# Optimization experiments

Hardware: AMD Instinct MI355X
Metric: run time of the kernel (lower is better)

## Reference

```python
import jax, jax.numpy as jnp
import numpy as np

B, L, D, NHEADS, P = 64, 256, 768, 8, 3
VOCAB, DEP, NLAYERS = 30522, 45, 2
LAM = 0.5


def _forward(src_mask, aspect_mask, lex, attention_mask,
             tok_emb, seg_emb, pool_w, pool_b, ln_a, ln_b,
             dep_emb, fc1_w, fc1_b, fc2_w, fc2_b,
             aq_w, aq_b, ak_w, ak_b, lq_w, lq_b, lk_w, lk_b, root_w,
             gcn_w, gcn_b, fc3_w, fc3_b, cls_w, cls_b, vlin_w,
             text_bert_indices, bert_segments_ids, ori_tag, head):
    b, l = text_bert_indices.shape
    d = tok_emb.shape[1]
    dk = d // NHEADS
    NEG = jnp.float32(-1e30)
    # stand-in BERT encoder: token + segment embeddings, tanh pooler on [CLS]
    seq = tok_emb[text_bert_indices] + seg_emb[bert_segments_ids]
    pooled = jnp.tanh(seq[:, 0] @ pool_w + pool_b)
    # torch LayerNorm variant: unbiased std (ddof=1)
    mean = seq.mean(-1, keepdims=True)
    std = jnp.std(seq, axis=-1, keepdims=True, ddof=1)
    gcn_in = ln_a * (seq - mean) / (std + 1e-6) + ln_b
    # in-place fmask[:,0]=1 mutates src_mask storage in torch -> effective mask
    sm = src_mask.at[:, 0].set(1.0)
    # dependency-tag score -> per-token softmax -> scatter into [L,L] adjacency
    dep_h = jax.nn.relu(dep_emb[ori_tag] @ fc1_w + fc1_b)
    dep_s = (dep_h @ fc2_w + fc2_b)[..., 0]                      # [B,L]
    dep_feat = jax.nn.softmax(dep_s * sm + (1.0 - sm) * NEG, axis=1)
    to_idx = jnp.arange(1, l)
    fro = head[:, :l - 1]                                        # [B,L-1]
    b_idx = jnp.arange(b)[:, None]
    vals = dep_feat[:, :l - 1]
    dep_adj = jnp.ones((b, l, l), jnp.float32)
    dep_adj = dep_adj.at[b_idx, fro, to_idx[None, :]].set(vals)
    dep_adj = dep_adj.at[b_idx, to_idx[None, :], fro].set(vals)
    # multi-head attention-as-adjacency (returns softmax weights only)
    q = (gcn_in @ aq_w + aq_b).reshape(b, l, NHEADS, dk).transpose(0, 2, 1, 3)
    k = (gcn_in @ ak_w + ak_b).reshape(b, l, NHEADS, dk).transpose(0, 2, 1, 3)
    scores = jnp.einsum('bhqd,bhkd->bhqk', q, k) / (jnp.sqrt(jnp.float32(dk)) + 1e-9)
    scores = jnp.where(sm[:, None, None, :] == 0, jnp.float32(-1e9), scores)
    adj_ag = jax.nn.softmax(scores, axis=-1).mean(axis=1)        # [B,L,L]
    eye = jnp.eye(l, dtype=jnp.float32)
    adj_ag = (adj_ag * (1.0 - eye) + eye) * sm[:, :, None]
    # structured latent attention (stand-in for missing StructuredAtt):
    # masked bilinear attention biased by dep_adj + root attention loss
    q2 = gcn_in @ lq_w + lq_b
    k2 = gcn_in @ lk_w + lk_b
    lat = jnp.einsum('bqd,bkd->bqk', q2, k2) / jnp.sqrt(jnp.float32(d))
    lat = lat + dep_adj + (1.0 - sm)[:, None, :] * (-10000.0)
    adj_latent = jax.nn.softmax(lat, axis=-1)
    root_p = jax.nn.softmax((gcn_in @ root_w)[..., 0] * sm + (1.0 - sm) * NEG, axis=1)
    loss_root = -jnp.mean(jnp.log(jnp.sum(root_p * aspect_mask, axis=1) + 1e-9))
    adj_latent = (adj_latent * (1.0 - eye) + eye) * sm[:, :, None]
    # gated dual-adjacency GCN layers
    H_l = gcn_in
    I_sem = gcn_in
    for layer in range(gcn_w.shape[0]):
        g_l = jax.nn.sigmoid(H_l)
        I_sem = (adj_ag @ H_l) @ gcn_w[layer] + gcn_b[layer]
        I_lat = (adj_latent @ H_l) @ gcn_w[layer] + gcn_b[layer]
        g = jax.nn.sigmoid(I_lat)
        lam_g = LAM * g
        I_com = (1.0 - lam_g) * I_sem + lam_g * I_lat
        H_out = jax.nn.relu(I_com @ fc3_w + fc3_b)
        H_l = g_l * H_out + (1.0 - g_l) * H_l
    # readout
    asp_wn = aspect_mask.sum(axis=1, keepdims=True)              # [B,1]
    m3 = sm[:, :, None]
    h_l = H_l * m3
    h_sem = I_sem * m3
    beta = jnp.einsum('bqd,bkd->bqk', h_l, h_sem) / 1000.0
    attn_o = jax.nn.softmax(beta.sum(axis=1, keepdims=True), axis=2)  # [B,1,L]
    outputs = (attn_o @ I_sem)[:, 0]                             # [B,D]
    sem_pool = (I_sem * aspect_mask[:, :, None]).sum(axis=1) / (asp_wn + 1e-9)
    final = jnp.concatenate([outputs, sem_pool, pooled], axis=-1)  # [B,3D]
    logits = final @ cls_w + cls_b
    e = (H_l @ vlin_w)[..., 0]
    lw = jax.nn.softmax(e, axis=1) * 50.0
    lw = lw * sm.at[:, 0].set(0.0)
    lexicon_loss = jnp.mean((lw - lex) ** 2)
    return logits, loss_root, lexicon_loss


def setup_inputs() -> dict:
    key = jax.random.key(0)
    ks = jax.random.split(key, 24)
    s = 0.02
    n = lambda i, shape: jax.random.normal(ks[i], shape, dtype=jnp.float32) * s
    inp = {}
    inp['text_bert_indices'] = jax.random.randint(ks[0], (B, L), 0, VOCAB, dtype=jnp.int32)
    inp['bert_segments_ids'] = jnp.zeros((B, L), jnp.int32)
    inp['attention_mask'] = jnp.ones((B, L), jnp.float32)
    inp['src_mask'] = jnp.ones((B, L), jnp.float32)
    inp['aspect_mask'] = jax.random.randint(ks[1], (B, L), 0, 2).astype(jnp.float32)
    inp['lex'] = jax.random.uniform(ks[2], (B, L), dtype=jnp.float32)
    inp['ori_tag'] = jax.random.randint(ks[3], (B, L), 0, DEP, dtype=jnp.int32)
    inp['head'] = jax.random.randint(ks[4], (B, L), 0, L, dtype=jnp.int32)
    inp['tok_emb'] = n(5, (VOCAB, D)); inp['seg_emb'] = n(6, (2, D))
    inp['pool_w'] = n(7, (D, D)); inp['pool_b'] = jnp.zeros((D,), jnp.float32)
    inp['ln_a'] = jnp.ones((D,), jnp.float32); inp['ln_b'] = jnp.zeros((D,), jnp.float32)
    inp['dep_emb'] = n(8, (DEP, 300))
    inp['fc1_w'] = n(9, (300, 256)); inp['fc1_b'] = jnp.zeros((256,), jnp.float32)
    inp['fc2_w'] = n(10, (256, 1)); inp['fc2_b'] = jnp.zeros((1,), jnp.float32)
    inp['aq_w'] = n(11, (D, D)); inp['aq_b'] = jnp.zeros((D,), jnp.float32)
    inp['ak_w'] = n(12, (D, D)); inp['ak_b'] = jnp.zeros((D,), jnp.float32)
    inp['lq_w'] = n(13, (D, D)); inp['lq_b'] = jnp.zeros((D,), jnp.float32)
    inp['lk_w'] = n(14, (D, D)); inp['lk_b'] = jnp.zeros((D,), jnp.float32)
    inp['root_w'] = n(15, (D, 1))
    inp['gcn_w'] = n(16, (NLAYERS, D, D)); inp['gcn_b'] = jnp.zeros((NLAYERS, D), jnp.float32)
    inp['fc3_w'] = n(17, (D, D)); inp['fc3_b'] = jnp.zeros((D,), jnp.float32)
    inp['cls_w'] = n(18, (3 * D, P)); inp['cls_b'] = jnp.zeros((P,), jnp.float32)
    inp['vlin_w'] = n(19, (D, 1))
    return inp


def reference(text_bert_indices, bert_segments_ids, attention_mask, src_mask, aspect_mask, lex,
              ori_tag, head, tok_emb, seg_emb, pool_w, pool_b, ln_a, ln_b, dep_emb,
              fc1_w, fc1_b, fc2_w, fc2_b, aq_w, aq_b, ak_w, ak_b, lq_w, lq_b, lk_w, lk_b,
              root_w, gcn_w, gcn_b, fc3_w, fc3_b, cls_w, cls_b, vlin_w):
    return _forward(src_mask, aspect_mask, lex, attention_mask,
                    tok_emb, seg_emb, pool_w, pool_b, ln_a, ln_b,
                    dep_emb, fc1_w, fc1_b, fc2_w, fc2_b,
                    aq_w, aq_b, ak_w, ak_b, lq_w, lq_b, lk_w, lk_b, root_w,
                    gcn_w, gcn_b, fc3_w, fc3_b, cls_w, cls_b, vlin_w,
                    text_bert_indices, bert_segments_ids, ori_tag, head)
```

## Files before the change

kernel.cpp:

```cpp
#include <hip/hip_runtime.h>
#include <hip/hip_bf16.h>
#include <math.h>

#define DI __device__ __forceinline__

constexpr int cB = 64, cL = 256, cD = 768;
constexpr long BLD = (long)cB * cL * cD;
constexpr long BLL = (long)cB * cL * cL;
constexpr long cLL = (long)cL * cL;
constexpr long cLD = (long)cL * cD;

typedef __attribute__((ext_vector_type(8))) short b8;
typedef __attribute__((ext_vector_type(4))) float f4;

DI float wsum(float v) {
#pragma unroll
  for (int o = 32; o > 0; o >>= 1) v += __shfl_down(v, o, 64);
  return v;
}
DI float wsum_all(float v) {
#pragma unroll
  for (int m = 32; m > 0; m >>= 1) v += __shfl_xor(v, m, 64);
  return v;
}
DI float wmax_all(float v) {
#pragma unroll
  for (int m = 32; m > 0; m >>= 1) v = fmaxf(v, __shfl_xor(v, m, 64));
  return v;
}
DI float wmaxr(float v) {
#pragma unroll
  for (int o = 32; o > 0; o >>= 1) v = fmaxf(v, __shfl_down(v, o, 64));
  return v;
}
DI float blockSum(float v) {
  __shared__ float sh[4];
  v = wsum(v);
  __syncthreads();
  if ((threadIdx.x & 63) == 0) sh[threadIdx.x >> 6] = v;
  __syncthreads();
  return sh[0] + sh[1] + sh[2] + sh[3];
}
DI float blockMax(float v) {
  __shared__ float sh[4];
  v = wmaxr(v);
  __syncthreads();
  if ((threadIdx.x & 63) == 0) sh[threadIdx.x >> 6] = v;
  __syncthreads();
  return fmaxf(fmaxf(sh[0], sh[1]), fmaxf(sh[2], sh[3]));
}
DI float sigf(float x) { return 1.f / (1.f + expf(-x)); }

template <int OBF, int RELU, int BIAS, int EPI>
__global__ __launch_bounds__(256, 2) void bgemm(
    const __hip_bfloat16* __restrict__ A, const __hip_bfloat16* __restrict__ BT,
    void* __restrict__ Cv, const float* __restrict__ bias,
    float* __restrict__ auxf, __hip_bfloat16* __restrict__ auxb,
    int K, int lda, int ldb, int ldc,
    int zshift, int zmask, long sA1, long sA2, long sB1, long sB2, long sC,
    int czdiv) {
  __shared__ __hip_bfloat16 Asp[4 * 129 * 8];
  __shared__ __hip_bfloat16 Bsp[4 * 129 * 8];
  int z = blockIdx.z;
  A += (long)(z >> zshift) * sA1 + (long)(z & zmask) * sA2;
  BT += (long)(z >> zshift) * sB1 + (long)(z & zmask) * sB2;
  int tid = threadIdx.x;
  int lane = tid & 63, w = tid >> 6;
  int wr = w >> 1, wc = w & 1;
  int l16 = lane & 15, q = lane >> 4;
  int m0 = blockIdx.y << 7, n0 = blockIdx.x << 7;

  int fm = tid >> 2, fq = tid & 3;
  const __hip_bfloat16* Ap0 = A + (long)(m0 + fm) * lda + fq * 8;
  const __hip_bfloat16* Ap1 = A + (long)(m0 + fm + 64) * lda + fq * 8;
  const __hip_bfloat16* Bp0 = BT + (long)(n0 + fm) * ldb + fq * 8;
  const __hip_bfloat16* Bp1 = BT + (long)(n0 + fm + 64) * ldb + fq * 8;
  __hip_bfloat16* Aw0 = &Asp[(fq * 129 + fm) * 8];
  __hip_bfloat16* Aw1 = &Asp[(fq * 129 + fm + 64) * 8];
  __hip_bfloat16* Bw0 = &Bsp[(fq * 129 + fm) * 8];
  __hip_bfloat16* Bw1 = &Bsp[(fq * 129 + fm + 64) * 8];

  f4 acc[4][4];
#pragma unroll
  for (int i = 0; i < 4; i++)
#pragma unroll
    for (int j = 0; j < 4; j++) acc[i][j] = (f4){0.f, 0.f, 0.f, 0.f};

  b8 pa0 = *(const b8*)Ap0, pa1 = *(const b8*)Ap1;
  b8 pb0 = *(const b8*)Bp0, pb1 = *(const b8*)Bp1;
  for (int k0 = 0; k0 < K; k0 += 32) {
    __syncthreads();
    *(b8*)Aw0 = pa0; *(b8*)Aw1 = pa1;
    *(b8*)Bw0 = pb0; *(b8*)Bw1 = pb1;
    __syncthreads();
    int k1 = k0 + 32;
    if (k1 < K) {
      pa0 = *(const b8*)(Ap0 + k1); pa1 = *(const b8*)(Ap1 + k1);
      pb0 = *(const b8*)(Bp0 + k1); pb1 = *(const b8*)(Bp1 + k1);
    }
    b8 af[4], bf[4];
#pragma unroll
    for (int i = 0; i < 4; i++)
      af[i] = *(const b8*)&Asp[(q * 129 + wr * 64 + i * 16 + l16) * 8];
#pragma unroll
    for (int j = 0; j < 4; j++)
      bf[j] = *(const b8*)&Bsp[(q * 129 + wc * 64 + j * 16 + l16) * 8];
#pragma unroll
    for (int i = 0; i < 4; i++)
#pragma unroll
      for (int j = 0; j < 4; j++)
        acc[i][j] = __builtin_amdgcn_mfma_f32_16x16x32_bf16(af[i], bf[j], acc[i][j], 0, 0, 0);
  }
  if (EPI == 4) {
#pragma unroll
    for (int j = 0; j < 4; j++) {
      int n = n0 + wc * 64 + j * 16 + l16;
#pragma unroll
      for (int i = 0; i < 4; i++) {
        int m = m0 + wr * 64 + i * 16 + (q << 2);
        __hip_bfloat16 t4[4];
#pragma unroll
        for (int r = 0; r < 4; r++) t4[r] = __float2bfloat16(acc[i][j][r]);
        long bidx = (long)(m >> 8) * sC + (long)n * cL + (m & 255);
        *(uint2*)&((__hip_bfloat16*)Cv)[bidx] = *(uint2*)t4;
      }
    }
    return;
  }
  long cz = (long)(z >> czdiv) * sC;
#pragma unroll
  for (int j = 0; j < 4; j++) {
    int n = n0 + wc * 64 + j * 16 + l16;
    float bv = BIAS ? bias[n] : 0.f;
#pragma unroll
    for (int i = 0; i < 4; i++) {
#pragma unroll
      for (int r = 0; r < 4; r++) {
        int m = m0 + wr * 64 + i * 16 + q * 4 + r;
        long idx = cz + (long)m * ldc + n;
        float v = acc[i][j][r] + bv;
        if (EPI == 0) {
          if (RELU) v = fmaxf(v, 0.f);
          if (OBF)
            ((__hip_bfloat16*)Cv)[idx] = __float2bfloat16(v);
          else
            ((float*)Cv)[idx] = v;
        } else if (EPI == 3) {
          atomicAdd(&((float*)Cv)[idx], v);
        } else {
          v = fmaxf(v, 0.f);
          float h = auxf[idx];
          float g = sigf(h);
          float o = h + g * (v - h);
          auxf[idx] = o;
          auxb[idx] = __float2bfloat16(o);
        }
      }
    }
  }
}

__global__ __launch_bounds__(256, 2) void bgemm_dual(
    const __hip_bfloat16* __restrict__ A1g, const __hip_bfloat16* __restrict__ A2g,
    const __hip_bfloat16* __restrict__ BTg, float* __restrict__ IsemF,
    __hip_bfloat16* __restrict__ Icb, const float* __restrict__ bias,
    int write_isem) {
  __shared__ __hip_bfloat16 A1sp[4 * 129 * 8];
  __shared__ __hip_bfloat16 A2sp[4 * 129 * 8];
  __shared__ __hip_bfloat16 Bsp[4 * 129 * 8];
  int z = blockIdx.z;
  const __hip_bfloat16* A1 = A1g + (long)z * cLL;
  const __hip_bfloat16* A2 = A2g + (long)z * cLL;
  const __hip_bfloat16* BT = BTg + (long)z * cLD;
  int tid = threadIdx.x;
  int lane = tid & 63, w = tid >> 6;
  int wr = w >> 1, wc = w & 1;
  int l16 = lane & 15, q = lane >> 4;
  int m0 = blockIdx.y << 7, n0 = blockIdx.x << 7;

  int fm = tid >> 2, fq = tid & 3;
  const __hip_bfloat16* A1p0 = A1 + (long)(m0 + fm) * cL + fq * 8;
  const __hip_bfloat16* A1p1 = A1p0 + 64L * cL;
  const __hip_bfloat16* A2p0 = A2 + (long)(m0 + fm) * cL + fq * 8;
  const __hip_bfloat16* A2p1 = A2p0 + 64L * cL;
  const __hip_bfloat16* Bp0 = BT + (long)(n0 + fm) * cL + fq * 8;
  const __hip_bfloat16* Bp1 = Bp0 + 64L * cL;
  __hip_bfloat16* w10 = &A1sp[(fq * 129 + fm) * 8];
  __hip_bfloat16* w11 = &A1sp[(fq * 129 + fm + 64) * 8];
  __hip_bfloat16* w20 = &A2sp[(fq * 129 + fm) * 8];
  __hip_bfloat16* w21 = &A2sp[(fq * 129 + fm + 64) * 8];
  __hip_bfloat16* wb0 = &Bsp[(fq * 129 + fm) * 8];
  __hip_bfloat16* wb1 = &Bsp[(fq * 129 + fm + 64) * 8];

  f4 ac1[4][4], ac2[4][4];
#pragma unroll
  for (int i = 0; i < 4; i++)
#pragma unroll
    for (int j = 0; j < 4; j++) {
      ac1[i][j] = (f4){0.f, 0.f, 0.f, 0.f};
      ac2[i][j] = (f4){0.f, 0.f, 0.f, 0.f};
    }

  b8 p10 = *(const b8*)A1p0, p11 = *(const b8*)A1p1;
  b8 p20 = *(const b8*)A2p0, p21 = *(const b8*)A2p1;
  b8 pb0 = *(const b8*)Bp0, pb1 = *(const b8*)Bp1;
  for (int k0 = 0; k0 < cL; k0 += 32) {
    __syncthreads();
    *(b8*)w10 = p10; *(b8*)w11 = p11;
    *(b8*)w20 = p20; *(b8*)w21 = p21;
    *(b8*)wb0 = pb0; *(b8*)wb1 = pb1;
    __syncthreads();
    int k1 = k0 + 32;
    if (k1 < cL) {
      p10 = *(const b8*)(A1p0 + k1); p11 = *(const b8*)(A1p1 + k1);
      p20 = *(const b8*)(A2p0 + k1); p21 = *(const b8*)(A2p1 + k1);
      pb0 = *(const b8*)(Bp0 + k1); pb1 = *(const b8*)(Bp1 + k1);
    }
    b8 a1f[4], a2f[4], bf[4];
#pragma unroll
    for (int i = 0; i < 4; i++) {
      a1f[i] = *(const b8*)&A1sp[(q * 129 + wr * 64 + i * 16 + l16) * 8];
      a2f[i] = *(const b8*)&A2sp[(q * 129 + wr * 64 + i * 16 + l16) * 8];
    }
#pragma unroll
    for (int j = 0; j < 4; j++)
      bf[j] = *(const b8*)&Bsp[(q * 129 + wc * 64 + j * 16 + l16) * 8];
#pragma unroll
    for (int i = 0; i < 4; i++)
#pragma unroll
      for (int j = 0; j < 4; j++) {
        ac1[i][j] = __builtin_amdgcn_mfma_f32_16x16x32_bf16(a1f[i], bf[j], ac1[i][j], 0, 0, 0);
        ac2[i][j] = __builtin_amdgcn_mfma_f32_16x16x32_bf16(a2f[i], bf[j], ac2[i][j], 0, 0, 0);
      }
  }
  long cz = (long)z * cLD;
#pragma unroll
  for (int j = 0; j < 4; j++) {
    int n = n0 + wc * 64 + j * 16 + l16;
    float bv = bias[n];
#pragma unroll
    for (int i = 0; i < 4; i++) {
#pragma unroll
      for (int r = 0; r < 4; r++) {
        int m = m0 + wr * 64 + i * 16 + q * 4 + r;
        long idx = cz + (long)m * cD + n;
        float is = ac1[i][j][r] + bv;
        float il = ac2[i][j][r] + bv;
        float g = 0.5f * sigf(il);
        Icb[idx] = __float2bfloat16(is + g * (il - is));
        if (write_isem) IsemF[idx] = is;
      }
    }
  }
}

__global__ void k_wconv7(const float* __restrict__ s0, const float* __restrict__ s1,
                         const float* __restrict__ s2, const float* __restrict__ s3,
                         const float* __restrict__ s4, const float* __restrict__ s5,
                         const float* __restrict__ s6, __hip_bfloat16* __restrict__ dst) {
  const float* srcs[7] = {s0, s1, s2, s3, s4, s5, s6};
  const float* src = srcs[blockIdx.z];
  __hip_bfloat16* d = dst + (long)blockIdx.z * cD * cD;
  __shared__ float t[32][33];
  int k0 = blockIdx.x * 32, n0 = blockIdx.y * 32;
  int tx = threadIdx.x, ty = threadIdx.y;
#pragma unroll
  for (int i = 0; i < 32; i += 8) t[ty + i][tx] = src[(long)(k0 + ty + i) * cD + n0 + tx];
  __syncthreads();
#pragma unroll
  for (int i = 0; i < 32; i += 8)
    d[(long)(n0 + ty + i) * cD + k0 + tx] = __float2bfloat16(t[tx][ty + i]);
}

__global__ __launch_bounds__(256) void k_gcnin(
    const int* __restrict__ tbi, const int* __restrict__ bsi,
    const float* __restrict__ tok, const float* __restrict__ seg,
    const float* __restrict__ ln_a, const float* __restrict__ ln_b,
    const float* __restrict__ root_w,
    float* __restrict__ gcn_in, __hip_bfloat16* __restrict__ gib,
    float* __restrict__ x64, float* __restrict__ e1) {
  long bl = blockIdx.x;
  int t = tbi[bl], s = bsi[bl];
  const float* tr = tok + (long)t * cD;
  const float* sr = seg + (long)s * cD;
  float x[3];
  float ls = 0.f;
#pragma unroll
  for (int i = 0; i < 3; i++) {
    int d = threadIdx.x + (i << 8);
    x[i] = tr[d] + sr[d];
    ls += x[i];
  }
  if ((bl & 255) == 0) {
#pragma unroll
    for (int i = 0; i < 3; i++) x64[(bl >> 8) * cD + threadIdx.x + (i << 8)] = x[i];
  }
  float mean = blockSum(ls) * (1.f / 768.f);
  float lv = 0.f;
#pragma unroll
  for (int i = 0; i < 3; i++) { float c = x[i] - mean; lv += c * c; }
  float var = blockSum(lv) * (1.f / 767.f);
  float inv = 1.f / (sqrtf(var) + 1e-6f);
  float rdot = 0.f;
#pragma unroll
  for (int i = 0; i < 3; i++) {
    int d = threadIdx.x + (i << 8);
    float v = ln_a[d] * (x[i] - mean) * inv + ln_b[d];
    gcn_in[bl * cD + d] = v;
    gib[bl * cD + d] = __float2bfloat16(v);
    rdot += v * root_w[d];
  }
  float tot = blockSum(rdot);
  if (threadIdx.x == 0) e1[bl] = tot;
}

__global__ __launch_bounds__(256) void k_pool1(
    const float* __restrict__ x64, const float* __restrict__ pw,
    float* __restrict__ pacc) {
  __shared__ float pws[48][256];
  __shared__ float xs[16][48];
  int i0 = blockIdx.x * 48, j0 = blockIdx.y * 256, b0 = blockIdx.z * 16;
  for (int r = 0; r < 48; r++) pws[r][threadIdx.x] = pw[(long)(i0 + r) * cD + j0 + threadIdx.x];
  for (int idx = threadIdx.x; idx < 16 * 48; idx += 256)
    xs[idx / 48][idx % 48] = x64[(long)(b0 + idx / 48) * cD + i0 + idx % 48];
  __syncthreads();
  int j = threadIdx.x;
  for (int b = 0; b < 16; b++) {
    float acc = 0.f;
#pragma unroll 8
    for (int i = 0; i < 48; i++) acc += xs[b][i] * pws[i][j];
    atomicAdd(&pacc[(long)(b0 + b) * cD + j0 + j], acc);
  }
}
__global__ __launch_bounds__(256) void k_pool2(
    const float* __restrict__ pacc, const float* __restrict__ pb,
    float* __restrict__ pooled) {
  int b = blockIdx.x;
#pragma unroll
  for (int c = 0; c < 3; c++) {
    int j = (c << 8) + threadIdx.x;
    pooled[(long)b * cD + j] = tanhf(pacc[(long)b * cD + j] + pb[j]);
  }
}

__global__ __launch_bounds__(256) void k_s45(
    const float* __restrict__ dep_emb, const float* __restrict__ fc1w,
    const float* __restrict__ fc1b, const float* __restrict__ fc2w,
    const float* __restrict__ fc2b, float* __restrict__ s45) {
  int t = blockIdx.x;
  __shared__ float e[300];
  for (int i = threadIdx.x; i < 300; i += 256) e[i] = dep_emb[t * 300 + i];
  __syncthreads();
  int j = threadIdx.x;
  float h = fc1b[j];
  for (int i = 0; i < 300; i++) h += e[i] * fc1w[i * 256 + j];
  h = fmaxf(h, 0.f);
  float tot = blockSum(h * fc2w[j]);
  if (threadIdx.x == 0) s45[t] = tot + fc2b[0];
}

__global__ __launch_bounds__(256) void k_depfeat(
    const int* __restrict__ ori, const float* __restrict__ src_mask,
    const float* __restrict__ s45, float* __restrict__ dep_feat) {
  int b = blockIdx.x, l = threadIdx.x;
  float smv = (l == 0) ? 1.f : src_mask[b * cL + l];
  float sc = s45[ori[b * cL + l]] * smv + (1.f - smv) * (-1e30f);
  float mx = blockMax(sc);
  float ex = expf(sc - mx);
  float sum = blockSum(ex);
  dep_feat[b * cL + l] = ex / sum;
}

__global__ void k_bcat(const float* __restrict__ a, const float* __restrict__ b,
                       const float* __restrict__ c, const float* __restrict__ d,
                       float* __restrict__ o) {
  int i = blockIdx.x * 256 + threadIdx.x;
  float v = (i < 768) ? a[i] : (i < 1536) ? b[i - 768] : (i < 2304) ? c[i - 1536] : d[i - 2304];
  o[i] = v;
}

__global__ __launch_bounds__(256) void k_adjag_sm(
    const __hip_bfloat16* __restrict__ scores, const float* __restrict__ src_mask,
    __hip_bfloat16* __restrict__ adjag) {
  int b = blockIdx.x >> 8, i = blockIdx.x & 255;
  int tid = threadIdx.x, wave = tid >> 6, lane = tid & 63;
  __shared__ float accs[4][256];
  const float scale = 1.f / (sqrtf(96.f) + 1e-9f);
  float smj[4], acc[4];
#pragma unroll
  for (int c = 0; c < 4; c++) {
    int j = c * 64 + lane;
    smj[c] = (j == 0) ? 1.f : src_mask[b * cL + j];
    acc[c] = 0.f;
  }
  for (int hh = 0; hh < 2; hh++) {
    int h = wave * 2 + hh;
    const __hip_bfloat16* row = scores + (((long)(b * 8 + h)) * cL + i) * cL;
    float s[4], m = -1e30f;
#pragma unroll
    for (int c = 0; c < 4; c++) {
      s[c] = (smj[c] == 0.f) ? -1e9f : __bfloat162float(row[c * 64 + lane]) * scale;
      m = fmaxf(m, s[c]);
    }
    m = wmax_all(m);
    float es = 0.f;
#pragma unroll
    for (int c = 0; c < 4; c++) { s[c] = expf(s[c] - m); es += s[c]; }
    es = wsum_all(es);
    float inv = 1.f / es;
#pragma unroll
    for (int c = 0; c < 4; c++) acc[c] += s[c] * inv;
  }
#pragma unroll
  for (int c = 0; c < 4; c++) accs[wave][c * 64 + lane] = acc[c];
  __syncthreads();
  int j = tid;
  float tot = accs[0][j] + accs[1][j] + accs[2][j] + accs[3][j];
  float smi = (i == 0) ? 1.f : src_mask[b * cL + i];
  float v = (j == i) ? 1.f : tot * 0.125f;
  adjag[((long)b * cL + i) * cL + j] = __float2bfloat16(v * smi);
}

__global__ __launch_bounds__(256) void k_adjlat_sm(
    const float* __restrict__ latsc, const int* __restrict__ head,
    const float* __restrict__ df, const float* __restrict__ src_mask,
    __hip_bfloat16* __restrict__ adjlat) {
  int b = blockIdx.x >> 8, i = blockIdx.x & 255;
  int j = threadIdx.x;
  float smj = (j == 0) ? 1.f : src_mask[b * cL + j];
  float dep = 1.f;
  if (j >= 1 && head[b * cL + j - 1] == i) dep = df[b * cL + j - 1];
  if (i >= 1 && j == head[b * cL + i - 1]) dep = df[b * cL + i - 1];
  float s = latsc[((long)b * cL + i) * cL + j] * (1.f / sqrtf(768.f)) +
            dep + (1.f - smj) * (-10000.f);
  float mx = blockMax(s);
  float ex = expf(s - mx);
  float sum = blockSum(ex);
  float p = ex / sum;
  float smi = (i == 0) ? 1.f : src_mask[b * cL + i];
  adjlat[((long)b * cL + i) * cL + j] = __float2bfloat16(((j == i) ? 1.f : p) * smi);
}

__global__ __launch_bounds__(256) void k_rowdot(
    const float* __restrict__ X, const float* __restrict__ w, long wstride,
    float* __restrict__ e) {
  int r = blockIdx.x * 4 + (threadIdx.x >> 6);
  int lane = threadIdx.x & 63;
  const float4* row = (const float4*)(X + (long)r * cD);
  const float4* wp = (const float4*)(w + (long)(r >> 8) * wstride);
  float s = 0.f;
#pragma unroll
  for (int c = 0; c < 3; c++) {
    int idx = c * 64 + lane;
    float4 a = row[idx], b = wp[idx];
    s += a.x * b.x + a.y * b.y + a.z * b.z + a.w * b.w;
  }
  s = wsum(s);
  if (lane == 0) e[r] = s;
}

__global__ __launch_bounds__(256) void k_root2(
    const float* __restrict__ e1, const float* __restrict__ src_mask,
    const float* __restrict__ aspect_mask, float* __restrict__ out_loss) {
  int b = blockIdx.x, l = threadIdx.x;
  float r = e1[b * cL + l];
  float smv = (l == 0) ? 1.f : src_mask[b * cL + l];
  float sc = r * smv + (1.f - smv) * (-1e30f);
  float mx = blockMax(sc);
  float ex = expf(sc - mx);
  float sum = blockSum(ex);
  float p = ex / sum;
  float tot = blockSum(p * aspect_mask[b * cL + l]);
  if (l == 0) atomicAdd(out_loss, -logf(tot + 1e-9f) * (1.f / 64.f));
}

__global__ __launch_bounds__(256) void k_lex2(
    const float* __restrict__ e2, const float* __restrict__ src_mask,
    const float* __restrict__ lex, float* __restrict__ out_loss) {
  int b = blockIdx.x, l = threadIdx.x;
  float e = e2[b * cL + l];
  float mx = blockMax(e);
  float ex = expf(e - mx);
  float sum = blockSum(ex);
  float mult = (l == 0) ? 0.f : src_mask[b * cL + l];
  float lw = ex / sum * 50.f * mult;
  float d2 = lw - lex[b * cL + l];
  float tot = blockSum(d2 * d2);
  if (l == 0) atomicAdd(out_loss, tot * (1.f / (64.f * 256.f)));
}

__global__ __launch_bounds__(256) void k_hl(
    const float* __restrict__ H, const float* __restrict__ src_mask,
    float* __restrict__ hlsum) {
  int b = blockIdx.z, d = (blockIdx.y << 8) + threadIdx.x, l0 = blockIdx.x * 32;
  float acc = 0.f;
  for (int l = l0; l < l0 + 32; l++) {
    float smv = (l == 0) ? 1.f : src_mask[b * cL + l];
    acc += H[((long)b * cL + l) * cD + d] * smv;
  }
  atomicAdd(&hlsum[(long)b * cD + d], acc);
}

__global__ __launch_bounds__(256) void k_attnw(
    const float* __restrict__ sraw, const float* __restrict__ src_mask,
    const float* __restrict__ am, float* __restrict__ wgt, float* __restrict__ asum) {
  int b = blockIdx.x, k = threadIdx.x;
  float smk = (k == 0) ? 1.f : src_mask[b * cL + k];
  float s = sraw[b * cL + k] * smk * 0.001f;
  float mx = blockMax(s);
  float ex = expf(s - mx);
  float sum = blockSum(ex);
  wgt[b * cL + k] = ex / sum;
  float a = blockSum(am[b * cL + k]);
  if (k == 0) asum[b] = a;
}

__global__ __launch_bounds__(256) void k_wsum(
    const float* __restrict__ Isem, const float* __restrict__ wgt,
    const float* __restrict__ am, float* __restrict__ outputs,
    float* __restrict__ sempool) {
  int b = blockIdx.z, d = (blockIdx.y << 8) + threadIdx.x, l0 = blockIdx.x * 32;
  float accO = 0.f, accS = 0.f;
  for (int l = l0; l < l0 + 32; l++) {
    float v = Isem[((long)b * cL + l) * cD + d];
    accO += wgt[b * cL + l] * v;
    accS += am[b * cL + l] * v;
  }
  atomicAdd(&outputs[(long)b * cD + d], accO);
  atomicAdd(&sempool[(long)b * cD + d], accS);
}

__global__ __launch_bounds__(256) void k_logits(
    const float* __restrict__ outputs, const float* __restrict__ sempool,
    const float* __restrict__ pooled, const float* __restrict__ asum,
    const float* __restrict__ cw, const float* __restrict__ cb,
    float* __restrict__ out) {
  int b = blockIdx.x;
  float inv = 1.f / (asum[b] + 1e-9f);
  float a0 = 0.f, a1 = 0.f, a2 = 0.f;
  for (int i = threadIdx.x; i < 3 * cD; i += 256) {
    float f = (i < cD) ? outputs[(long)b * cD + i]
              : (i < 2 * cD) ? sempool[(long)b * cD + i - cD] * inv
                             : pooled[(long)b * cD + i - 2 * cD];
    a0 += f * cw[i * 3 + 0];
    a1 += f * cw[i * 3 + 1];
    a2 += f * cw[i * 3 + 2];
  }
  a0 = blockSum(a0);
  a1 = blockSum(a1);
  a2 = blockSum(a2);
  if (threadIdx.x == 0) {
    out[b * 3 + 0] = a0 + cb[0];
    out[b * 3 + 1] = a1 + cb[1];
    out[b * 3 + 2] = a2 + cb[2];
  }
}

extern "C" void kernel_launch(void* const* d_in, const int* in_sizes, int n_in,
                              void* d_out, int out_size, void* d_ws, size_t ws_size,
                              hipStream_t stream) {
  const int* tbi = (const int*)d_in[0];
  const int* bsi = (const int*)d_in[1];
  const float* src_mask = (const float*)d_in[3];
  const float* aspect_mask = (const float*)d_in[4];
  const float* lex = (const float*)d_in[5];
  const int* ori = (const int*)d_in[6];
  const int* head = (const int*)d_in[7];
  const float* tok_emb = (const float*)d_in[8];
  const float* seg_emb = (const float*)d_in[9];
  const float* pool_w = (const float*)d_in[10];
  const float* pool_b = (const float*)d_in[11];
  const float* ln_a = (const float*)d_in[12];
  const float* ln_b = (const float*)d_in[13];
  const float* dep_emb = (const float*)d_in[14];
  const float* fc1_w = (const float*)d_in[15];
  const float* fc1_b = (const float*)d_in[16];
  const float* fc2_w = (const float*)d_in[17];
  const float* fc2_b = (const float*)d_in[18];
  const float* aq_w = (const float*)d_in[19];
  const float* aq_b = (const float*)d_in[20];
  const float* ak_w = (const float*)d_in[21];
  const float* ak_b = (const float*)d_in[22];
  const float* lq_w = (const float*)d_in[23];
  const float* lq_b = (const float*)d_in[24];
  const float* lk_w = (const float*)d_in[25];
  const float* lk_b = (const float*)d_in[26];
  const float* root_w = (const float*)d_in[27];
  const float* gcn_w = (const float*)d_in[28];
  const float* gcn_b = (const float*)d_in[29];
  const float* fc3_w = (const float*)d_in[30];
  const float* fc3_b = (const float*)d_in[31];
  const float* cls_w = (const float*)d_in[32];
  const float* cls_b = (const float*)d_in[33];
  const float* vlin_w = (const float*)d_in[34];

  float* out = (float*)d_out;
  float* ws = (float*)d_ws;
  float* gcnH = ws;
  float* Isem = gcnH + BLD;
  float* depfeat = Isem + BLD;
  float* s45 = depfeat + cB * cL;
  float* pooled = s45 + 64;
  float* x64 = pooled + cB * cD;
  float* hlsum = x64 + cB * cD;
  float* outputs = hlsum + cB * cD;
  float* sempool = outputs + cB * cD;
  float* pacc = sempool + cB * cD;
  float* e1 = pacc + cB * cD;
  float* e2 = e1 + cB * cL;
  float* sraw = e2 + cB * cL;
  float* wgt = sraw + cB * cL;
  float* asum = wgt + cB * cL;
  float* catb = asum + 64;
  float* latsc = Isem;
  __hip_bfloat16* gib = (__hip_bfloat16*)(catb + 3072);
  __hip_bfloat16* qkb = gib + BLD;
  __hip_bfloat16* scores = qkb + 4 * BLD;
  __hip_bfloat16* adjag_b = scores + 8 * BLL;
  __hip_bfloat16* adjlat_b = adjag_b + BLL;
  __hip_bfloat16* wbt = adjlat_b + BLL;
  __hip_bfloat16* HWbT = qkb + BLD;
  __hip_bfloat16* Icb = qkb + 2 * BLD;

  hipMemsetAsync((char*)d_out + 192 * sizeof(float), 0, 2 * sizeof(float), stream);
  hipMemsetAsync(hlsum, 0, 4 * cB * cD * sizeof(float), stream);
  hipMemsetAsync(latsc, 0, BLL * sizeof(float), stream);

  k_gcnin<<<cB * cL, 256, 0, stream>>>(tbi, bsi, tok_emb, seg_emb, ln_a, ln_b,
                                       root_w, gcnH, gib, x64, e1);
  k_s45<<<45, 256, 0, stream>>>(dep_emb, fc1_w, fc1_b, fc2_w, fc2_b, s45);
  k_depfeat<<<cB, 256, 0, stream>>>(ori, src_mask, s45, depfeat);
  k_pool1<<<dim3(16, 3, 4), 256, 0, stream>>>(x64, pool_w, pacc);
  k_pool2<<<cB, 256, 0, stream>>>(pacc, pool_b, pooled);
  k_bcat<<<12, 256, 0, stream>>>(aq_b, ak_b, lq_b, lk_b, catb);
  k_wconv7<<<dim3(24, 24, 7), dim3(32, 8), 0, stream>>>(
      aq_w, ak_w, lq_w, lk_w, gcn_w, gcn_w + (long)cD * cD, fc3_w, wbt);

  const long DD = (long)cD * cD;
  const long LD = cLD, LL = cLL;
  const long LP = (long)cL * 3072;

  bgemm<1, 0, 1, 0><<<dim3(24, 128, 1), 256, 0, stream>>>(
      gib, wbt, qkb, catb, nullptr, nullptr, cD, cD, cD, 3072,
      0, 0, 0, 0, 0, 0, 0, 0);

  bgemm<1, 0, 0, 0><<<dim3(2, 2, cB * 8), 256, 0, stream>>>(
      qkb, qkb + 768, scores, nullptr, nullptr, nullptr,
      96, 3072, 3072, cL, 3, 7, LP, 96, LP, 96, LL, 0);
  k_adjag_sm<<<cB * cL, 256, 0, stream>>>(scores, src_mask, adjag_b);

  bgemm<0, 0, 0, 3><<<dim3(2, 2, cB * 2), 256, 0, stream>>>(
      qkb + 1536, qkb + 2304, latsc, nullptr, nullptr, nullptr,
      384, 3072, 3072, cL, 1, 1, LP, 384, LP, 384, LL, 1);
  k_adjlat_sm<<<cB * cL, 256, 0, stream>>>(latsc, head, depfeat, src_mask, adjlat_b);

  k_root2<<<cB, 256, 0, stream>>>(e1, src_mask, aspect_mask, out + 192);

  for (int layer = 0; layer < 2; layer++) {
    const float* bb = gcn_b + (long)layer * cD;
    bgemm<1, 0, 0, 4><<<dim3(6, 128, 1), 256, 0, stream>>>(
        gib, wbt + (4 + layer) * DD, HWbT, nullptr, nullptr, nullptr,
        cD, cD, cD, cD, 0, 0, 0, 0, 0, 0, LD, 0);
    bgemm_dual<<<dim3(6, 2, cB), 256, 0, stream>>>(
        adjag_b, adjlat_b, HWbT, Isem, Icb, bb, layer == 1 ? 1 : 0);
    bgemm<0, 1, 1, 2><<<dim3(6, 128, 1), 256, 0, stream>>>(
        Icb, wbt + 6 * DD, nullptr, fc3_b, gcnH, gib,
        cD, cD, cD, cD, 0, 0, 0, 0, 0, 0, 0, 0);
  }

  k_hl<<<dim3(8, 3, cB), 256, 0, stream>>>(gcnH, src_mask, hlsum);
  k_rowdot<<<cB * cL / 4, 256, 0, stream>>>(Isem, hlsum, cD, sraw);
  k_attnw<<<cB, 256, 0, stream>>>(sraw, src_mask, aspect_mask, wgt, asum);
  k_wsum<<<dim3(8, 3, cB), 256, 0, stream>>>(Isem, wgt, aspect_mask, outputs, sempool);
  k_logits<<<cB, 256, 0, stream>>>(outputs, sempool, pooled, asum, cls_w, cls_b, out);
  k_rowdot<<<cB * cL / 4, 256, 0, stream>>>(gcnH, vlin_w, 0, e2);
  k_lex2<<<cB, 256, 0, stream>>>(e2, src_mask, lex, out + 193);
}
```

Measured before the change: 899.1 us.

## Use direct global-to-LDS double buffering in GEMMs and fuse small epilogue kernels

The bf16 GEMM kernels now use global_load_lds into double-buffered shared memory, so each k-step needs one barrier instead of two and register staging goes away. The last fc3 GEMM epilogue now also computes the masked hidden-sum and the vlin row dot products with atomics, which removes the k_hl kernel and a k_rowdot pass over gcnH. The latent-score split-K writes two partial slabs that are summed in the softmax, replacing atomicAdd and the large memset. The pooler tanh moves into the logits kernel, and bias concatenation merges into the weight-conversion launch. These changes double LDS use, which may reduce occupancy, and add atomic traffic in the epilogue.

```diff
diff --git a/kernel.cpp b/kernel.cpp
--- a/kernel.cpp
+++ b/kernel.cpp
@@ -12,6 +12,12 @@
 
 typedef __attribute__((ext_vector_type(8))) short b8;
 typedef __attribute__((ext_vector_type(4))) float f4;
+
+DI void gll16(const __hip_bfloat16* g, __hip_bfloat16* l) {
+  __builtin_amdgcn_global_load_lds(
+      (const __attribute__((address_space(1))) unsigned int*)g,
+      (__attribute__((address_space(3))) unsigned int*)l, 16, 0, 0);
+}
 
 DI float wsum(float v) {
 #pragma unroll
@@ -56,11 +62,14 @@
     const __hip_bfloat16* __restrict__ A, const __hip_bfloat16* __restrict__ BT,
     void* __restrict__ Cv, const float* __restrict__ bias,
     float* __restrict__ auxf, __hip_bfloat16* __restrict__ auxb,
+    const float* __restrict__ smk, const float* __restrict__ vlin,
+    float* __restrict__ hlsum, float* __restrict__ e2,
     int K, int lda, int ldb, int ldc,
-    int zshift, int zmask, long sA1, long sA2, long sB1, long sB2, long sC,
-    int czdiv) {
-  __shared__ __hip_bfloat16 Asp[4 * 129 * 8];
-  __shared__ __hip_bfloat16 Bsp[4 * 129 * 8];
+    int zshift, int zmask, long sA1, long sA2, long sB1, long sB2,
+    long sC, long sC2) {
+  constexpr int BUF = 4 * 129 * 8;
+  __shared__ __align__(16) __hip_bfloat16 Asp[2 * BUF];
+  __shared__ __align__(16) __hip_bfloat16 Bsp[2 * BUF];
   int z = blockIdx.z;
   A += (long)(z >> zshift) * sA1 + (long)(z & zmask) * sA2;
   BT += (long)(z >> zshift) * sB1 + (long)(z & zmask) * sB2;
@@ -70,15 +79,11 @@
   int l16 = lane & 15, q = lane >> 4;
   int m0 = blockIdx.y << 7, n0 = blockIdx.x << 7;
 
-  int fm = tid >> 2, fq = tid & 3;
-  const __hip_bfloat16* Ap0 = A + (long)(m0 + fm) * lda + fq * 8;
-  const __hip_bfloat16* Ap1 = A + (long)(m0 + fm + 64) * lda + fq * 8;
-  const __hip_bfloat16* Bp0 = BT + (long)(n0 + fm) * ldb + fq * 8;
-  const __hip_bfloat16* Bp1 = BT + (long)(n0 + fm + 64) * ldb + fq * 8;
-  __hip_bfloat16* Aw0 = &Asp[(fq * 129 + fm) * 8];
-  __hip_bfloat16* Aw1 = &Asp[(fq * 129 + fm + 64) * 8];
-  __hip_bfloat16* Bw0 = &Bsp[(fq * 129 + fm) * 8];
-  __hip_bfloat16* Bw1 = &Bsp[(fq * 129 + fm + 64) * 8];
+  const __hip_bfloat16* Ag0 = A + (long)(m0 + lane) * lda + w * 8;
+  const __hip_bfloat16* Ag1 = Ag0 + 64L * lda;
+  const __hip_bfloat16* Bg0 = BT + (long)(n0 + lane) * ldb + w * 8;
+  const __hip_bfloat16* Bg1 = Bg0 + 64L * ldb;
+  int sb = (w * 129) * 8;
 
   f4 acc[4][4];
 #pragma unroll
@@ -86,31 +91,38 @@
 #pragma unroll
     for (int j = 0; j < 4; j++) acc[i][j] = (f4){0.f, 0.f, 0.f, 0.f};
 
-  b8 pa0 = *(const b8*)Ap0, pa1 = *(const b8*)Ap1;
-  b8 pb0 = *(const b8*)Bp0, pb1 = *(const b8*)Bp1;
+  gll16(Ag0, &Asp[sb]);
+  gll16(Ag1, &Asp[sb + 64 * 8]);
+  gll16(Bg0, &Bsp[sb]);
+  gll16(Bg1, &Bsp[sb + 64 * 8]);
+
+  int buf = 0;
   for (int k0 = 0; k0 < K; k0 += 32) {
     __syncthreads();
-    *(b8*)Aw0 = pa0; *(b8*)Aw1 = pa1;
-    *(b8*)Bw0 = pb0; *(b8*)Bw1 = pb1;
-    __syncthreads();
+    int bo = buf * BUF;
+    b8 af[4], bf[4];
+#pragma unroll
+    for (int i = 0; i < 4; i++)
+      af[i] = *(const b8*)&Asp[bo + (q * 129 + wr * 64 + i * 16 + l16) * 8];
+#pragma unroll
+    for (int j = 0; j < 4; j++)
+      bf[j] = *(const b8*)&Bsp[bo + (q * 129 + wc * 64 + j * 16 + l16) * 8];
     int k1 = k0 + 32;
     if (k1 < K) {
-      pa0 = *(const b8*)(Ap0 + k1); pa1 = *(const b8*)(Ap1 + k1);
-      pb0 = *(const b8*)(Bp0 + k1); pb1 = *(const b8*)(Bp1 + k1);
-    }
-    b8 af[4], bf[4];
-#pragma unroll
-    for (int i = 0; i < 4; i++)
-      af[i] = *(const b8*)&Asp[(q * 129 + wr * 64 + i * 16 + l16) * 8];
-#pragma unroll
-    for (int j = 0; j < 4; j++)
-      bf[j] = *(const b8*)&Bsp[(q * 129 + wc * 64 + j * 16 + l16) * 8];
+      int no = (buf ^ 1) * BUF;
+      gll16(Ag0 + k1, &Asp[no + sb]);
+      gll16(Ag1 + k1, &Asp[no + sb + 64 * 8]);
+      gll16(Bg0 + k1, &Bsp[no + sb]);
+      gll16(Bg1 + k1, &Bsp[no + sb + 64 * 8]);
+    }
 #pragma unroll
     for (int i = 0; i < 4; i++)
 #pragma unroll
       for (int j = 0; j < 4; j++)
         acc[i][j] = __builtin_amdgcn_mfma_f32_16x16x32_bf16(af[i], bf[j], acc[i][j], 0, 0, 0);
-  }
+    buf ^= 1;
+  }
+
   if (EPI == 4) {
 #pragma unroll
     for (int j = 0; j < 4; j++) {
@@ -127,7 +139,61 @@
     }
     return;
   }
-  long cz = (long)(z >> czdiv) * sC;
+  if (EPI == 5) {
+    int b = m0 >> 8;
+#pragma unroll
+    for (int j = 0; j < 4; j++) {
+      int n = n0 + wc * 64 + j * 16 + l16;
+      float bv = bias[n];
+#pragma unroll
+      for (int i = 0; i < 4; i++)
+#pragma unroll
+        for (int r = 0; r < 4; r++) {
+          int m = m0 + wr * 64 + i * 16 + q * 4 + r;
+          long idx = (long)m * ldc + n;
+          float v = fmaxf(acc[i][j][r] + bv, 0.f);
+          float h = auxf[idx];
+          float g = sigf(h);
+          float o = h + g * (v - h);
+          auxf[idx] = o;
+          auxb[idx] = __float2bfloat16(o);
+          acc[i][j][r] = o;
+        }
+    }
+    float vl[4];
+#pragma unroll
+    for (int j = 0; j < 4; j++) vl[j] = vlin[n0 + wc * 64 + j * 16 + l16];
+#pragma unroll
+    for (int i = 0; i < 4; i++)
+#pragma unroll
+      for (int r = 0; r < 4; r++) {
+        float pe = acc[i][0][r] * vl[0] + acc[i][1][r] * vl[1] +
+                   acc[i][2][r] * vl[2] + acc[i][3][r] * vl[3];
+        pe += __shfl_xor(pe, 1, 64);
+        pe += __shfl_xor(pe, 2, 64);
+        pe += __shfl_xor(pe, 4, 64);
+        pe += __shfl_xor(pe, 8, 64);
+        if (l16 == 0) atomicAdd(&e2[m0 + wr * 64 + i * 16 + q * 4 + r], pe);
+      }
+#pragma unroll
+    for (int j = 0; j < 4; j++) {
+      float ph = 0.f;
+#pragma unroll
+      for (int i = 0; i < 4; i++)
+#pragma unroll
+        for (int r = 0; r < 4; r++) {
+          int m = m0 + wr * 64 + i * 16 + q * 4 + r;
+          int l = m & 255;
+          float smv = (l == 0) ? 1.f : smk[b * cL + l];
+          ph += acc[i][j][r] * smv;
+        }
+      ph += __shfl_xor(ph, 16, 64);
+      ph += __shfl_xor(ph, 32, 64);
+      if (q == 0) atomicAdd(&hlsum[(long)b * cD + n0 + wc * 64 + j * 16 + l16], ph);
+    }
+    return;
+  }
+  long cz = (long)(z >> zshift) * sC + (long)(z & zmask) * sC2;
 #pragma unroll
   for (int j = 0; j < 4; j++) {
     int n = n0 + wc * 64 + j * 16 + l16;
@@ -145,8 +211,6 @@
             ((__hip_bfloat16*)Cv)[idx] = __float2bfloat16(v);
           else
             ((float*)Cv)[idx] = v;
-        } else if (EPI == 3) {
-          atomicAdd(&((float*)Cv)[idx], v);
         } else {
           v = fmaxf(v, 0.f);
           float h = auxf[idx];
@@ -165,9 +229,10 @@
     const __hip_bfloat16* __restrict__ BTg, float* __restrict__ IsemF,
     __hip_bfloat16* __restrict__ Icb, const float* __restrict__ bias,
     int write_isem) {
-  __shared__ __hip_bfloat16 A1sp[4 * 129 * 8];
-  __shared__ __hip_bfloat16 A2sp[4 * 129 * 8];
-  __shared__ __hip_bfloat16 Bsp[4 * 129 * 8];
+  constexpr int BUF = 4 * 129 * 8;
+  __shared__ __align__(16) __hip_bfloat16 A1sp[2 * BUF];
+  __shared__ __align__(16) __hip_bfloat16 A2sp[2 * BUF];
+  __shared__ __align__(16) __hip_bfloat16 Bsp[2 * BUF];
   int z = blockIdx.z;
   const __hip_bfloat16* A1 = A1g + (long)z * cLL;
   const __hip_bfloat16* A2 = A2g + (long)z * cLL;
@@ -178,19 +243,13 @@
   int l16 = lane & 15, q = lane >> 4;
   int m0 = blockIdx.y << 7, n0 = blockIdx.x << 7;
 
-  int fm = tid >> 2, fq = tid & 3;
-  const __hip_bfloat16* A1p0 = A1 + (long)(m0 + fm) * cL + fq * 8;
-  const __hip_bfloat16* A1p1 = A1p0 + 64L * cL;
-  const __hip_bfloat16* A2p0 = A2 + (long)(m0 + fm) * cL + fq * 8;
-  const __hip_bfloat16* A2p1 = A2p0 + 64L * cL;
-  const __hip_bfloat16* Bp0 = BT + (long)(n0 + fm) * cL + fq * 8;
-  const __hip_bfloat16* Bp1 = Bp0 + 64L * cL;
-  __hip_bfloat16* w10 = &A1sp[(fq * 129 + fm) * 8];
-  __hip_bfloat16* w11 = &A1sp[(fq * 129 + fm + 64) * 8];
-  __hip_bfloat16* w20 = &A2sp[(fq * 129 + fm) * 8];
-  __hip_bfloat16* w21 = &A2sp[(fq * 129 + fm + 64) * 8];
-  __hip_bfloat16* wb0 = &Bsp[(fq * 129 + fm) * 8];
-  __hip_bfloat16* wb1 = &Bsp[(fq * 129 + fm + 64) * 8];
+  const __hip_bfloat16* A1g0 = A1 + (long)(m0 + lane) * cL + w * 8;
+  const __hip_bfloat16* A1g1 = A1g0 + 64L * cL;
+  const __hip_bfloat16* A2g0 = A2 + (long)(m0 + lane) * cL + w * 8;
+  const __hip_bfloat16* A2g1 = A2g0 + 64L * cL;
+  const __hip_bfloat16* Bg0 = BT + (long)(n0 + lane) * cL + w * 8;
+  const __hip_bfloat16* Bg1 = Bg0 + 64L * cL;
+  int sb = (w * 129) * 8;
 
   f4 ac1[4][4], ac2[4][4];
 #pragma unroll
@@ -201,30 +260,36 @@
       ac2[i][j] = (f4){0.f, 0.f, 0.f, 0.f};
     }
 
-  b8 p10 = *(const b8*)A1p0, p11 = *(const b8*)A1p1;
-  b8 p20 = *(const b8*)A2p0, p21 = *(const b8*)A2p1;
-  b8 pb0 = *(const b8*)Bp0, pb1 = *(const b8*)Bp1;
+  gll16(A1g0, &A1sp[sb]);
+  gll16(A1g1, &A1sp[sb + 64 * 8]);
+  gll16(A2g0, &A2sp[sb]);
+  gll16(A2g1, &A2sp[sb + 64 * 8]);
+  gll16(Bg0, &Bsp[sb]);
+  gll16(Bg1, &Bsp[sb + 64 * 8]);
+
+  int buf = 0;
   for (int k0 = 0; k0 < cL; k0 += 32) {
     __syncthreads();
-    *(b8*)w10 = p10; *(b8*)w11 = p11;
-    *(b8*)w20 = p20; *(b8*)w21 = p21;
-    *(b8*)wb0 = pb0; *(b8*)wb1 = pb1;
-    __syncthreads();
+    int bo = buf * BUF;
+    b8 a1f[4], a2f[4], bf[4];
+#pragma unroll
+    for (int i = 0; i < 4; i++) {
+      a1f[i] = *(const b8*)&A1sp[bo + (q * 129 + wr * 64 + i * 16 + l16) * 8];
+      a2f[i] = *(const b8*)&A2sp[bo + (q * 129 + wr * 64 + i * 16 + l16) * 8];
+    }
+#pragma unroll
+    for (int j = 0; j < 4; j++)
+      bf[j] = *(const b8*)&Bsp[bo + (q * 129 + wc * 64 + j * 16 + l16) * 8];
     int k1 = k0 + 32;
     if (k1 < cL) {
-      p10 = *(const b8*)(A1p0 + k1); p11 = *(const b8*)(A1p1 + k1);
-      p20 = *(const b8*)(A2p0 + k1); p21 = *(const b8*)(A2p1 + k1);
-      pb0 = *(const b8*)(Bp0 + k1); pb1 = *(const b8*)(Bp1 + k1);
-    }
-    b8 a1f[4], a2f[4], bf[4];
-#pragma unroll
-    for (int i = 0; i < 4; i++) {
-      a1f[i] = *(const b8*)&A1sp[(q * 129 + wr * 64 + i * 16 + l16) * 8];
-      a2f[i] = *(const b8*)&A2sp[(q * 129 + wr * 64 + i * 16 + l16) * 8];
-    }
-#pragma unroll
-    for (int j = 0; j < 4; j++)
-      bf[j] = *(const b8*)&Bsp[(q * 129 + wc * 64 + j * 16 + l16) * 8];
+      int no = (buf ^ 1) * BUF;
+      gll16(A1g0 + k1, &A1sp[no + sb]);
+      gll16(A1g1 + k1, &A1sp[no + sb + 64 * 8]);
+      gll16(A2g0 + k1, &A2sp[no + sb]);
+      gll16(A2g1 + k1, &A2sp[no + sb + 64 * 8]);
+      gll16(Bg0 + k1, &Bsp[no + sb]);
+      gll16(Bg1 + k1, &Bsp[no + sb + 64 * 8]);
+    }
 #pragma unroll
     for (int i = 0; i < 4; i++)
 #pragma unroll
@@ -232,6 +297,7 @@
         ac1[i][j] = __builtin_amdgcn_mfma_f32_16x16x32_bf16(a1f[i], bf[j], ac1[i][j], 0, 0, 0);
         ac2[i][j] = __builtin_amdgcn_mfma_f32_16x16x32_bf16(a2f[i], bf[j], ac2[i][j], 0, 0, 0);
       }
+    buf ^= 1;
   }
   long cz = (long)z * cLD;
 #pragma unroll
@@ -254,13 +320,26 @@
   }
 }
 
-__global__ void k_wconv7(const float* __restrict__ s0, const float* __restrict__ s1,
+__global__ void k_wconv8(const float* __restrict__ s0, const float* __restrict__ s1,
                          const float* __restrict__ s2, const float* __restrict__ s3,
                          const float* __restrict__ s4, const float* __restrict__ s5,
-                         const float* __restrict__ s6, __hip_bfloat16* __restrict__ dst) {
+                         const float* __restrict__ s6,
+                         const float* __restrict__ b0, const float* __restrict__ b1,
+                         const float* __restrict__ b2, const float* __restrict__ b3,
+                         __hip_bfloat16* __restrict__ dst, float* __restrict__ catb) {
+  int zz = blockIdx.z;
+  if (zz == 7) {
+    if (blockIdx.y == 0 && blockIdx.x < 12) {
+      int i = blockIdx.x * 256 + threadIdx.y * 32 + threadIdx.x;
+      float v = (i < 768) ? b0[i] : (i < 1536) ? b1[i - 768]
+                : (i < 2304) ? b2[i - 1536] : b3[i - 2304];
+      catb[i] = v;
+    }
+    return;
+  }
   const float* srcs[7] = {s0, s1, s2, s3, s4, s5, s6};
-  const float* src = srcs[blockIdx.z];
-  __hip_bfloat16* d = dst + (long)blockIdx.z * cD * cD;
+  const float* src = srcs[zz];
+  __hip_bfloat16* d = dst + (long)zz * cD * cD;
   __shared__ float t[32][33];
   int k0 = blockIdx.x * 32, n0 = blockIdx.y * 32;
   int tx = threadIdx.x, ty = threadIdx.y;
@@ -332,16 +411,6 @@
     atomicAdd(&pacc[(long)(b0 + b) * cD + j0 + j], acc);
   }
 }
-__global__ __launch_bounds__(256) void k_pool2(
-    const float* __restrict__ pacc, const float* __restrict__ pb,
-    float* __restrict__ pooled) {
-  int b = blockIdx.x;
-#pragma unroll
-  for (int c = 0; c < 3; c++) {
-    int j = (c << 8) + threadIdx.x;
-    pooled[(long)b * cD + j] = tanhf(pacc[(long)b * cD + j] + pb[j]);
-  }
-}
 
 __global__ __launch_bounds__(256) void k_s45(
     const float* __restrict__ dep_emb, const float* __restrict__ fc1w,
@@ -371,14 +440,6 @@
   dep_feat[b * cL + l] = ex / sum;
 }
 
-__global__ void k_bcat(const float* __restrict__ a, const float* __restrict__ b,
-                       const float* __restrict__ c, const float* __restrict__ d,
-                       float* __restrict__ o) {
-  int i = blockIdx.x * 256 + threadIdx.x;
-  float v = (i < 768) ? a[i] : (i < 1536) ? b[i - 768] : (i < 2304) ? c[i - 1536] : d[i - 2304];
-  o[i] = v;
-}
-
 __global__ __launch_bounds__(256) void k_adjag_sm(
     const __hip_bfloat16* __restrict__ scores, const float* __restrict__ src_mask,
     __hip_bfloat16* __restrict__ adjag) {
@@ -427,18 +488,19 @@
     __hip_bfloat16* __restrict__ adjlat) {
   int b = blockIdx.x >> 8, i = blockIdx.x & 255;
   int j = threadIdx.x;
+  long idx = ((long)b * cL + i) * cL + j;
   float smj = (j == 0) ? 1.f : src_mask[b * cL + j];
   float dep = 1.f;
   if (j >= 1 && head[b * cL + j - 1] == i) dep = df[b * cL + j - 1];
   if (i >= 1 && j == head[b * cL + i - 1]) dep = df[b * cL + i - 1];
-  float s = latsc[((long)b * cL + i) * cL + j] * (1.f / sqrtf(768.f)) +
+  float s = (latsc[idx] + latsc[BLL + idx]) * (1.f / sqrtf(768.f)) +
             dep + (1.f - smj) * (-10000.f);
   float mx = blockMax(s);
   float ex = expf(s - mx);
   float sum = blockSum(ex);
   float p = ex / sum;
   float smi = (i == 0) ? 1.f : src_mask[b * cL + i];
-  adjlat[((long)b * cL + i) * cL + j] = __float2bfloat16(((j == i) ? 1.f : p) * smi);
+  adjlat[idx] = __float2bfloat16(((j == i) ? 1.f : p) * smi);
 }
 
 __global__ __launch_bounds__(256) void k_rowdot(
@@ -489,18 +551,6 @@
   if (l == 0) atomicAdd(out_loss, tot * (1.f / (64.f * 256.f)));
 }
 
-__global__ __launch_bounds__(256) void k_hl(
-    const float* __restrict__ H, const float* __restrict__ src_mask,
-    float* __restrict__ hlsum) {
-  int b = blockIdx.z, d = (blockIdx.y << 8) + threadIdx.x, l0 = blockIdx.x * 32;
-  float acc = 0.f;
-  for (int l = l0; l < l0 + 32; l++) {
-    float smv = (l == 0) ? 1.f : src_mask[b * cL + l];
-    acc += H[((long)b * cL + l) * cD + d] * smv;
-  }
-  atomicAdd(&hlsum[(long)b * cD + d], acc);
-}
-
 __global__ __launch_bounds__(256) void k_attnw(
     const float* __restrict__ sraw, const float* __restrict__ src_mask,
     const float* __restrict__ am, float* __restrict__ wgt, float* __restrict__ asum) {
@@ -532,16 +582,16 @@
 
 __global__ __launch_bounds__(256) void k_logits(
     const float* __restrict__ outputs, const float* __restrict__ sempool,
-    const float* __restrict__ pooled, const float* __restrict__ asum,
-    const float* __restrict__ cw, const float* __restrict__ cb,
-    float* __restrict__ out) {
+    const float* __restrict__ pacc, const float* __restrict__ pb,
+    const float* __restrict__ asum, const float* __restrict__ cw,
+    const float* __restrict__ cb, float* __restrict__ out) {
   int b = blockIdx.x;
   float inv = 1.f / (asum[b] + 1e-9f);
   float a0 = 0.f, a1 = 0.f, a2 = 0.f;
   for (int i = threadIdx.x; i < 3 * cD; i += 256) {
     float f = (i < cD) ? outputs[(long)b * cD + i]
               : (i < 2 * cD) ? sempool[(long)b * cD + i - cD] * inv
-                             : pooled[(long)b * cD + i - 2 * cD];
+                             : tanhf(pacc[(long)b * cD + i - 2 * cD] + pb[i - 2 * cD]);
     a0 += f * cw[i * 3 + 0];
     a1 += f * cw[i * 3 + 1];
     a2 += f * cw[i * 3 + 2];
@@ -600,15 +650,14 @@
   float* Isem = gcnH + BLD;
   float* depfeat = Isem + BLD;
   float* s45 = depfeat + cB * cL;
-  float* pooled = s45 + 64;
-  float* x64 = pooled + cB * cD;
+  float* x64 = s45 + 64;
   float* hlsum = x64 + cB * cD;
   float* outputs = hlsum + cB * cD;
   float* sempool = outputs + cB * cD;
   float* pacc = sempool + cB * cD;
-  float* e1 = pacc + cB * cD;
-  float* e2 = e1 + cB * cL;
-  float* sraw = e2 + cB * cL;
+  float* e2 = pacc + cB * cD;
+  float* e1 = e2 + cB * cL;
+  float* sraw = e1 + cB * cL;
   float* wgt = sraw + cB * cL;
   float* asum = wgt + cB * cL;
   float* catb = asum + 64;
@@ -623,35 +672,33 @@
   __hip_bfloat16* Icb = qkb + 2 * BLD;
 
   hipMemsetAsync((char*)d_out + 192 * sizeof(float), 0, 2 * sizeof(float), stream);
-  hipMemsetAsync(hlsum, 0, 4 * cB * cD * sizeof(float), stream);
-  hipMemsetAsync(latsc, 0, BLL * sizeof(float), stream);
+  hipMemsetAsync(hlsum, 0, (4 * cB * cD + cB * cL) * sizeof(float), stream);
 
   k_gcnin<<<cB * cL, 256, 0, stream>>>(tbi, bsi, tok_emb, seg_emb, ln_a, ln_b,
                                        root_w, gcnH, gib, x64, e1);
   k_s45<<<45, 256, 0, stream>>>(dep_emb, fc1_w, fc1_b, fc2_w, fc2_b, s45);
   k_depfeat<<<cB, 256, 0, stream>>>(ori, src_mask, s45, depfeat);
   k_pool1<<<dim3(16, 3, 4), 256, 0, stream>>>(x64, pool_w, pacc);
-  k_pool2<<<cB, 256, 0, stream>>>(pacc, pool_b, pooled);
-  k_bcat<<<12, 256, 0, stream>>>(aq_b, ak_b, lq_b, lk_b, catb);
-  k_wconv7<<<dim3(24, 24, 7), dim3(32, 8), 0, stream>>>(
-      aq_w, ak_w, lq_w, lk_w, gcn_w, gcn_w + (long)cD * cD, fc3_w, wbt);
+  k_wconv8<<<dim3(24, 24, 8), dim3(32, 8), 0, stream>>>(
+      aq_w, ak_w, lq_w, lk_w, gcn_w, gcn_w + (long)cD * cD, fc3_w,
+      aq_b, ak_b, lq_b, lk_b, wbt, catb);
 
   const long DD = (long)cD * cD;
-  const long LD = cLD, LL = cLL;
+  const long LD = cLD;
   const long LP = (long)cL * 3072;
 
   bgemm<1, 0, 1, 0><<<dim3(24, 128, 1), 256, 0, stream>>>(
-      gib, wbt, qkb, catb, nullptr, nullptr, cD, cD, cD, 3072,
-      0, 0, 0, 0, 0, 0, 0, 0);
+      gib, wbt, qkb, catb, nullptr, nullptr, nullptr, nullptr, nullptr, nullptr,
+      cD, cD, cD, 3072, 0, 0, 0, 0, 0, 0, 0, 0);
 
   bgemm<1, 0, 0, 0><<<dim3(2, 2, cB * 8), 256, 0, stream>>>(
-      qkb, qkb + 768, scores, nullptr, nullptr, nullptr,
-      96, 3072, 3072, cL, 3, 7, LP, 96, LP, 96, LL, 0);
+      qkb, qkb + 768, scores, nullptr, nullptr, nullptr, nullptr, nullptr, nullptr, nullptr,
+      96, 3072, 3072, cL, 3, 7, LP, 96, LP, 96, 8 * cLL, cLL);
   k_adjag_sm<<<cB * cL, 256, 0, stream>>>(scores, src_mask, adjag_b);
 
-  bgemm<0, 0, 0, 3><<<dim3(2, 2, cB * 2), 256, 0, stream>>>(
-      qkb + 1536, qkb + 2304, latsc, nullptr, nullptr, nullptr,
-      384, 3072, 3072, cL, 1, 1, LP, 384, LP, 384, LL, 1);
+  bgemm<0, 0, 0, 0><<<dim3(2, 2, cB * 2), 256, 0, stream>>>(
+      qkb + 1536, qkb + 2304, latsc, nullptr, nullptr, nullptr, nullptr, nullptr, nullptr, nullptr,
+      384, 3072, 3072, cL, 1, 1, LP, 384, LP, 384, cLL, BLL);
   k_adjlat_sm<<<cB * cL, 256, 0, stream>>>(latsc, head, depfeat, src_mask, adjlat_b);
 
   k_root2<<<cB, 256, 0, stream>>>(e1, src_mask, aspect_mask, out + 192);
@@ -660,19 +707,25 @@
     const float* bb = gcn_b + (long)layer * cD;
     bgemm<1, 0, 0, 4><<<dim3(6, 128, 1), 256, 0, stream>>>(
         gib, wbt + (4 + layer) * DD, HWbT, nullptr, nullptr, nullptr,
+        nullptr, nullptr, nullptr, nullptr,
         cD, cD, cD, cD, 0, 0, 0, 0, 0, 0, LD, 0);
     bgemm_dual<<<dim3(6, 2, cB), 256, 0, stream>>>(
         adjag_b, adjlat_b, HWbT, Isem, Icb, bb, layer == 1 ? 1 : 0);
-    bgemm<0, 1, 1, 2><<<dim3(6, 128, 1), 256, 0, stream>>>(
-        Icb, wbt + 6 * DD, nullptr, fc3_b, gcnH, gib,
-        cD, cD, cD, cD, 0, 0, 0, 0, 0, 0, 0, 0);
-  }
-
-  k_hl<<<dim3(8, 3, cB), 256, 0, stream>>>(gcnH, src_mask, hlsum);
+    if (layer == 0)
+      bgemm<0, 1, 1, 2><<<dim3(6, 128, 1), 256, 0, stream>>>(
+          Icb, wbt + 6 * DD, nullptr, fc3_b, gcnH, gib,
+          nullptr, nullptr, nullptr, nullptr,
+          cD, cD, cD, cD, 0, 0, 0, 0, 0, 0, 0, 0);
+    else
+      bgemm<0, 1, 1, 5><<<dim3(6, 128, 1), 256, 0, stream>>>(
+          Icb, wbt + 6 * DD, nullptr, fc3_b, gcnH, gib,
+          src_mask, vlin_w, hlsum, e2,
+          cD, cD, cD, cD, 0, 0, 0, 0, 0, 0, 0, 0);
+  }
+
   k_rowdot<<<cB * cL / 4, 256, 0, stream>>>(Isem, hlsum, cD, sraw);
   k_attnw<<<cB, 256, 0, stream>>>(sraw, src_mask, aspect_mask, wgt, asum);
   k_wsum<<<dim3(8, 3, cB), 256, 0, stream>>>(Isem, wgt, aspect_mask, outputs, sempool);
-  k_logits<<<cB, 256, 0, stream>>>(outputs, sempool, pooled, asum, cls_w, cls_b, out);
-  k_rowdot<<<cB * cL / 4, 256, 0, stream>>>(gcnH, vlin_w, 0, e2);
+  k_logits<<<cB, 256, 0, stream>>>(outputs, sempool, pacc, pool_b, asum, cls_w, cls_b, out);
   k_lex2<<<cB, 256, 0, stream>>>(e2, src_mask, lex, out + 193);
 }
```

New measurement: 969.8 us. +7.9%, slower.
